# Kernel tuning notes

Measured on AMD Instinct MI355X. Metric: run time of the kernel, lower is better.

Reference implementation:

```python
import jax, jax.numpy as jnp
import numpy as np

# Deformable Conv v2 (modulated) config matching init_kwargs
KH, KW = 3, 3
STRIDE = (1, 1)
PAD = (1, 1)
DIL = (1, 1)


def _deform_conv2d(input, offset, mask, weight, bias):
    """Modulated deformable conv2d (DCNv2), deformable_groups=1.

    input:  [B, C, H, W]
    offset: [B, 2*K, Ho, Wo]  (y, x) interleaved per kernel tap
    mask:   [B, K, Ho, Wo]
    weight: [O, C, KH, KW]
    bias:   [O]
    """
    B, C, H, W = input.shape
    O = weight.shape[0]
    K = KH * KW
    sh, sw = STRIDE
    ph, pw = PAD
    dh, dw = DIL
    Ho = (H + 2 * ph - dh * (KH - 1) - 1) // sh + 1
    Wo = (W + 2 * pw - dw * (KW - 1) - 1) // sw + 1
    dt = input.dtype

    # Base sampling grid per kernel tap: [K, Ho, Wo] (broadcasted)
    ky, kx = jnp.meshgrid(jnp.arange(KH), jnp.arange(KW), indexing='ij')
    ky = ky.reshape(K).astype(dt)
    kx = kx.reshape(K).astype(dt)
    base_y = (jnp.arange(Ho, dtype=dt) * sh - ph)[None, :, None] + (ky * dh)[:, None, None]
    base_x = (jnp.arange(Wo, dtype=dt) * sw - pw)[None, None, :] + (kx * dw)[:, None, None]

    off = offset.reshape(B, K, 2, Ho, Wo)
    y = base_y[None] + off[:, :, 0]  # [B, K, Ho, Wo]
    x = base_x[None] + off[:, :, 1]

    y0 = jnp.floor(y)
    x0 = jnp.floor(x)
    wy = y - y0  # fractional parts
    wx = x - x0

    flat = input.reshape(B, C, H * W)

    def gather(yi, xi):
        # zero padding outside the image
        valid = ((yi >= 0) & (yi < H) & (xi >= 0) & (xi < W)).astype(dt)
        yc = jnp.clip(yi, 0, H - 1).astype(jnp.int32)
        xc = jnp.clip(xi, 0, W - 1).astype(jnp.int32)
        idx = (yc * W + xc).reshape(B, 1, K * Ho * Wo)
        v = jnp.take_along_axis(flat, jnp.broadcast_to(idx, (B, C, K * Ho * Wo)), axis=2)
        return v.reshape(B, C, K, Ho, Wo) * valid[:, None]

    g00 = gather(y0, x0)
    g01 = gather(y0, x0 + 1)
    g10 = gather(y0 + 1, x0)
    g11 = gather(y0 + 1, x0 + 1)

    wy = wy[:, None]  # [B, 1, K, Ho, Wo]
    wx = wx[:, None]
    val = (g00 * (1 - wy) * (1 - wx) + g01 * (1 - wy) * wx
           + g10 * wy * (1 - wx) + g11 * wy * wx)
    val = val * mask[:, None]  # modulation

    out = jnp.einsum('bckq,ock->boq', val.reshape(B, C, K, Ho * Wo),
                     weight.reshape(O, C, K))
    return out.reshape(B, O, Ho, Wo) + bias[None, :, None, None]


def setup_inputs() -> dict:
    key = jax.random.key(0)
    k1, k2, k3, k4, k5 = jax.random.split(key, 5)
    B, C, H, W = 8, 64, 96, 96
    O = 64
    K = KH * KW
    input = jax.random.normal(k1, (B, C, H, W), dtype=jnp.float32)
    offset = jax.random.normal(k2, (B, 2 * K, H, W), dtype=jnp.float32)
    mask = jax.random.uniform(k3, (B, K, H, W), dtype=jnp.float32)
    fan_in = C * KH * KW
    bound = 1.0 / np.sqrt(fan_in)
    weight = jax.random.uniform(k4, (O, C, KH, KW), minval=-bound, maxval=bound, dtype=jnp.float32)
    bias = jax.random.uniform(k5, (O,), minval=-bound, maxval=bound, dtype=jnp.float32)
    return {"input": input, "offset": offset, "mask": mask, "weight": weight, "bias": bias}


def reference(input, offset, mask, weight, bias):
    return _deform_conv2d(input, offset, mask, weight, bias)
```

## Files before the change

kernel.cpp:

```cpp
#include <hip/hip_runtime.h>
#include <stdint.h>

#define Hs 96
#define Ws 96
#define HW 9216

typedef _Float16 h2 __attribute__((ext_vector_type(2)));
typedef _Float16 f16x8 __attribute__((ext_vector_type(8)));
typedef float f32x4 __attribute__((ext_vector_type(4)));

__device__ __forceinline__ unsigned interp4(h2 w00, h2 w01, h2 w10, h2 w11,
                                            unsigned a, unsigned bq, unsigned c,
                                            unsigned d) {
  h2 r = w10 * __builtin_bit_cast(h2, c) + w11 * __builtin_bit_cast(h2, d);
  r = w01 * __builtin_bit_cast(h2, bq) + r;
  r = w00 * __builtin_bit_cast(h2, a) + r;
  return __builtin_bit_cast(unsigned, r);
}

__global__ __launch_bounds__(256) void k_prep(const float* __restrict__ in,
                                              _Float16* __restrict__ cl,
                                              const float* __restrict__ w,
                                              _Float16* __restrict__ wg) {
  __shared__ _Float16 lt[32 * 68];
  int tid = threadIdx.x;
  int blk = blockIdx.x;
  if (blk >= 2304) {
    int i = (blk - 2304) * 256 + tid;
    int o = i / 576;
    int r = i - o * 576;
    int t = r >> 6, c = r & 63;
    wg[((size_t)(t * 8 + (c >> 3)) * 64 + o) * 8 + (c & 7)] =
        (_Float16)w[(o * 64 + c) * 9 + t];
    return;
  }
  int xt = blk % 3;
  int rr = blk / 3;
  int y = rr % Hs;
  int b = rr / Hs;
  int x0 = xt * 32;
  {
    int xx = tid & 31, cc = tid >> 5;
    const float* src = in + (size_t)b * 64 * HW + y * Ws + x0 + xx;
#pragma unroll
    for (int i = 0; i < 8; ++i) {
      int c = cc * 8 + i;
      lt[xx * 68 + c] = (_Float16)src[(size_t)c * HW];
    }
  }
  __syncthreads();
  {
    int c4 = tid & 15, pg = tid >> 4;
    _Float16* dst = cl + ((size_t)(b * Hs + y) * Ws + x0) * 64 + c4 * 4;
#pragma unroll
    for (int i = 0; i < 2; ++i) {
      int x = pg * 2 + i;
      *(uint2*)(dst + (size_t)x * 64) = *(const uint2*)(lt + x * 68 + c4 * 4);
    }
  }
}

__global__ __launch_bounds__(256, 5) void k_fused(
    const _Float16* __restrict__ incl, const float* __restrict__ off,
    const float* __restrict__ msk, const _Float16* __restrict__ wg,
    const float* __restrict__ bias, float* __restrict__ out) {
  __shared__ unsigned preA[576];
  __shared__ uint4 preW[576];
  __shared__ uint4 Vb[2][64 * 9];

  int tid = threadIdx.x;
  int blk = blockIdx.x;
  int b = blk & 7;
  int q0 = (blk >> 3) * 64;

  for (int i = tid; i < 576; i += 256) {
    int t = i >> 6, p = i & 63;
    int q = q0 + p;
    int qy = (int)(((unsigned)q * 43691u) >> 22);
    int qx = q - qy * 96;
    int ty = t / 3, tx = t - ty * 3;
    float dy = off[(size_t)(b * 18 + 2 * t) * HW + q];
    float dx = off[(size_t)(b * 18 + 2 * t + 1) * HW + q];
    float mv = msk[(size_t)(b * 9 + t) * HW + q];
    float yf = (float)(qy - 1 + ty) + dy;
    float xf = (float)(qx - 1 + tx) + dx;
    float y0f = floorf(yf), x0f = floorf(xf);
    float wy = yf - y0f, wx = xf - x0f;
    int y0 = (int)y0f, x0i = (int)x0f;
    int y1 = y0 + 1, x1 = x0i + 1;
    bool yv0 = (y0 >= 0) && (y0 < Hs);
    bool yv1 = (y1 >= 0) && (y1 < Hs);
    bool xv0 = (x0i >= 0) && (x0i < Ws);
    bool xv1 = (x1 >= 0) && (x1 < Ws);
    int y0c = min(max(y0, 0), Hs - 1), y1c = min(max(y1, 0), Hs - 1);
    int x0c = min(max(x0i, 0), Ws - 1), x1c = min(max(x1, 0), Ws - 1);
    float omy = 1.f - wy, omx = 1.f - wx;
    float f00 = omy * omx * mv * ((yv0 && xv0) ? 1.f : 0.f);
    float f01 = omy * wx  * mv * ((yv0 && xv1) ? 1.f : 0.f);
    float f10 = wy  * omx * mv * ((yv1 && xv0) ? 1.f : 0.f);
    float f11 = wy  * wx  * mv * ((yv1 && xv1) ? 1.f : 0.f);
    preA[i] = ((unsigned)(b * HW + y0c * 96 + x0c) * 128u) |
              (unsigned)(x1c - x0c) | ((unsigned)(y1c - y0c) << 1);
    uint4 pw;
    pw.x = __builtin_bit_cast(unsigned, __builtin_amdgcn_cvt_pkrtz(f00, f00));
    pw.y = __builtin_bit_cast(unsigned, __builtin_amdgcn_cvt_pkrtz(f01, f01));
    pw.z = __builtin_bit_cast(unsigned, __builtin_amdgcn_cvt_pkrtz(f10, f10));
    pw.w = __builtin_bit_cast(unsigned, __builtin_amdgcn_cvt_pkrtz(f11, f11));
    preW[i] = pw;
  }
  __syncthreads();

  int j = tid & 7;
  int g = tid >> 3;
  int lane = tid & 63, wv = tid >> 6;
  int n16 = lane & 15, q4 = lane >> 4;
  const char* inb = (const char*)incl;
  const uint4* Ag = (const uint4*)wg;
  int arow = wv * 16 + n16;

  f32x4 acc[4];
#pragma unroll
  for (int pg = 0; pg < 4; ++pg) {
    f32x4 z = {0.f, 0.f, 0.f, 0.f};
    acc[pg] = z;
  }

  uint4 ga[2][4];
  uint4 afn0, afn1;

#define ISSUE_GATHERS(T)                                                     \
  _Pragma("unroll") for (int it = 0; it < 2; ++it) {                         \
    int gg = g + it * 32;                                                    \
    unsigned ax = preA[(T) * 64 + gg];                                       \
    int a00 = (int)(ax & ~127u) + j * 16;                                    \
    int a01 = a00 + ((ax & 1) << 7);                                         \
    int a10 = a00 + ((ax & 2) * 6144);                                       \
    int a11 = a10 + ((ax & 1) << 7);                                         \
    ga[it][0] = *(const uint4*)(inb + a00);                                  \
    ga[it][1] = *(const uint4*)(inb + a01);                                  \
    ga[it][2] = *(const uint4*)(inb + a10);                                  \
    ga[it][3] = *(const uint4*)(inb + a11);                                  \
  }

  ISSUE_GATHERS(0)
  afn0 = Ag[(size_t)((0 + q4) * 64 + arow)];
  afn1 = Ag[(size_t)((4 + q4) * 64 + arow)];

#pragma unroll
  for (int t = 0; t < 9; ++t) {
    int buf = t & 1;
    uint4 v0, v1;
#pragma unroll
    for (int it = 0; it < 2; ++it) {
      int gg = g + it * 32;
      uint4 pw = preW[t * 64 + gg];
      h2 w00 = __builtin_bit_cast(h2, pw.x);
      h2 w01 = __builtin_bit_cast(h2, pw.y);
      h2 w10 = __builtin_bit_cast(h2, pw.z);
      h2 w11 = __builtin_bit_cast(h2, pw.w);
      uint4 r;
      r.x = interp4(w00, w01, w10, w11, ga[it][0].x, ga[it][1].x, ga[it][2].x, ga[it][3].x);
      r.y = interp4(w00, w01, w10, w11, ga[it][0].y, ga[it][1].y, ga[it][2].y, ga[it][3].y);
      r.z = interp4(w00, w01, w10, w11, ga[it][0].z, ga[it][1].z, ga[it][2].z, ga[it][3].z);
      r.w = interp4(w00, w01, w10, w11, ga[it][0].w, ga[it][1].w, ga[it][2].w, ga[it][3].w);
      if (it == 0) v0 = r; else v1 = r;
    }
    uint4 afc0 = afn0, afc1 = afn1;
    Vb[buf][g * 9 + j] = v0;
    Vb[buf][(g + 32) * 9 + j] = v1;
    __syncthreads();
    if (t < 8) {
      ISSUE_GATHERS(t + 1)
      afn0 = Ag[(size_t)(((t + 1) * 8 + q4) * 64 + arow)];
      afn1 = Ag[(size_t)(((t + 1) * 8 + 4 + q4) * 64 + arow)];
    }
#pragma unroll
    for (int pg = 0; pg < 4; ++pg) {
      f16x8 b0 = __builtin_bit_cast(f16x8, Vb[buf][(pg * 16 + n16) * 9 + q4]);
      f16x8 b1 = __builtin_bit_cast(f16x8, Vb[buf][(pg * 16 + n16) * 9 + 4 + q4]);
      acc[pg] = __builtin_amdgcn_mfma_f32_16x16x32_f16(
          __builtin_bit_cast(f16x8, afc0), b0, acc[pg], 0, 0, 0);
      acc[pg] = __builtin_amdgcn_mfma_f32_16x16x32_f16(
          __builtin_bit_cast(f16x8, afc1), b1, acc[pg], 0, 0, 0);
    }
  }
#undef ISSUE_GATHERS

  int m0 = wv * 16 + q4 * 4;
  float bv[4];
#pragma unroll
  for (int r = 0; r < 4; ++r) bv[r] = bias[m0 + r];
#pragma unroll
  for (int pg = 0; pg < 4; ++pg) {
    int col = q0 + pg * 16 + n16;
    float* op = out + (size_t)b * 64 * HW + col;
#pragma unroll
    for (int r = 0; r < 4; ++r)
      op[(size_t)(m0 + r) * HW] = acc[pg][r] + bv[r];
  }
}

extern "C" void kernel_launch(void* const* d_in, const int* in_sizes, int n_in,
                              void* d_out, int out_size, void* d_ws, size_t ws_size,
                              hipStream_t stream) {
  const float* input = (const float*)d_in[0];
  const float* offset = (const float*)d_in[1];
  const float* mask = (const float*)d_in[2];
  const float* weight = (const float*)d_in[3];
  const float* bias = (const float*)d_in[4];
  float* out = (float*)d_out;

  _Float16* incl = (_Float16*)d_ws;
  _Float16* wg = (_Float16*)((char*)d_ws + 9437184);

  k_prep<<<dim3(2448), dim3(256), 0, stream>>>(input, incl, weight, wg);
  k_fused<<<dim3(1152), dim3(256), 0, stream>>>(incl, offset, mask, wg, bias, out);
}
```

Measured before the change: 100.4 us.

## Give each wave its own pixel tile to drop block-wide barriers in tap loop

```diff
diff --git a/kernel.cpp b/kernel.cpp
--- a/kernel.cpp
+++ b/kernel.cpp
@@ -66,7 +66,7 @@
     const float* __restrict__ bias, float* __restrict__ out) {
   __shared__ unsigned preA[576];
   __shared__ uint4 preW[576];
-  __shared__ uint4 Vb[2][64 * 9];
+  __shared__ uint4 Vw[4][16 * 9];
 
   int tid = threadIdx.x;
   int blk = blockIdx.x;
@@ -110,27 +110,25 @@
   }
   __syncthreads();
 
-  int j = tid & 7;
-  int g = tid >> 3;
   int lane = tid & 63, wv = tid >> 6;
   int n16 = lane & 15, q4 = lane >> 4;
+  int grp = lane >> 3, j = lane & 7;
+  int wvb = wv * 16;
   const char* inb = (const char*)incl;
   const uint4* Ag = (const uint4*)wg;
-  int arow = wv * 16 + n16;
 
   f32x4 acc[4];
 #pragma unroll
-  for (int pg = 0; pg < 4; ++pg) {
+  for (int mt = 0; mt < 4; ++mt) {
     f32x4 z = {0.f, 0.f, 0.f, 0.f};
-    acc[pg] = z;
+    acc[mt] = z;
   }
 
   uint4 ga[2][4];
-  uint4 afn0, afn1;
 
 #define ISSUE_GATHERS(T)                                                     \
   _Pragma("unroll") for (int it = 0; it < 2; ++it) {                         \
-    int gg = g + it * 32;                                                    \
+    int gg = wvb + grp + it * 8;                                             \
     unsigned ax = preA[(T) * 64 + gg];                                       \
     int a00 = (int)(ax & ~127u) + j * 16;                                    \
     int a01 = a00 + ((ax & 1) << 7);                                         \
@@ -143,17 +141,13 @@
   }
 
   ISSUE_GATHERS(0)
-  afn0 = Ag[(size_t)((0 + q4) * 64 + arow)];
-  afn1 = Ag[(size_t)((4 + q4) * 64 + arow)];
 
 #pragma unroll
   for (int t = 0; t < 9; ++t) {
-    int buf = t & 1;
     uint4 v0, v1;
 #pragma unroll
     for (int it = 0; it < 2; ++it) {
-      int gg = g + it * 32;
-      uint4 pw = preW[t * 64 + gg];
+      uint4 pw = preW[t * 64 + wvb + grp + it * 8];
       h2 w00 = __builtin_bit_cast(h2, pw.x);
       h2 w01 = __builtin_bit_cast(h2, pw.y);
       h2 w10 = __builtin_bit_cast(h2, pw.z);
@@ -165,38 +159,40 @@
       r.w = interp4(w00, w01, w10, w11, ga[it][0].w, ga[it][1].w, ga[it][2].w, ga[it][3].w);
       if (it == 0) v0 = r; else v1 = r;
     }
-    uint4 afc0 = afn0, afc1 = afn1;
-    Vb[buf][g * 9 + j] = v0;
-    Vb[buf][(g + 32) * 9 + j] = v1;
-    __syncthreads();
+    Vw[wv][grp * 9 + j] = v0;
+    Vw[wv][(grp + 8) * 9 + j] = v1;
     if (t < 8) {
       ISSUE_GATHERS(t + 1)
-      afn0 = Ag[(size_t)(((t + 1) * 8 + q4) * 64 + arow)];
-      afn1 = Ag[(size_t)(((t + 1) * 8 + 4 + q4) * 64 + arow)];
-    }
-#pragma unroll
-    for (int pg = 0; pg < 4; ++pg) {
-      f16x8 b0 = __builtin_bit_cast(f16x8, Vb[buf][(pg * 16 + n16) * 9 + q4]);
-      f16x8 b1 = __builtin_bit_cast(f16x8, Vb[buf][(pg * 16 + n16) * 9 + 4 + q4]);
-      acc[pg] = __builtin_amdgcn_mfma_f32_16x16x32_f16(
-          __builtin_bit_cast(f16x8, afc0), b0, acc[pg], 0, 0, 0);
-      acc[pg] = __builtin_amdgcn_mfma_f32_16x16x32_f16(
-          __builtin_bit_cast(f16x8, afc1), b1, acc[pg], 0, 0, 0);
+    }
+    uint4 a0[4], a1[4];
+#pragma unroll
+    for (int mt = 0; mt < 4; ++mt) {
+      a0[mt] = Ag[(size_t)((t * 8 + q4) * 64 + mt * 16 + n16)];
+      a1[mt] = Ag[(size_t)((t * 8 + 4 + q4) * 64 + mt * 16 + n16)];
+    }
+    uint4 b0q = Vw[wv][n16 * 9 + q4];
+    uint4 b1q = Vw[wv][n16 * 9 + 4 + q4];
+    __builtin_amdgcn_sched_barrier(0);
+#pragma unroll
+    for (int mt = 0; mt < 4; ++mt) {
+      acc[mt] = __builtin_amdgcn_mfma_f32_16x16x32_f16(
+          __builtin_bit_cast(f16x8, a0[mt]), __builtin_bit_cast(f16x8, b0q),
+          acc[mt], 0, 0, 0);
+      acc[mt] = __builtin_amdgcn_mfma_f32_16x16x32_f16(
+          __builtin_bit_cast(f16x8, a1[mt]), __builtin_bit_cast(f16x8, b1q),
+          acc[mt], 0, 0, 0);
     }
   }
 #undef ISSUE_GATHERS
 
-  int m0 = wv * 16 + q4 * 4;
-  float bv[4];
-#pragma unroll
-  for (int r = 0; r < 4; ++r) bv[r] = bias[m0 + r];
-#pragma unroll
-  for (int pg = 0; pg < 4; ++pg) {
-    int col = q0 + pg * 16 + n16;
-    float* op = out + (size_t)b * 64 * HW + col;
+  int colq = q0 + wvb + n16;
+  float* op = out + (size_t)b * 64 * HW + colq;
+#pragma unroll
+  for (int mt = 0; mt < 4; ++mt) {
+    f32x4 bv = *(const f32x4*)(bias + mt * 16 + q4 * 4);
 #pragma unroll
     for (int r = 0; r < 4; ++r)
-      op[(size_t)(m0 + r) * HW] = acc[pg][r] + bv[r];
+      op[(size_t)(mt * 16 + q4 * 4 + r) * HW] = acc[mt][r] + bv[r];
   }
 }
 
```

After: 130.4 us. 29.9% more time.
